# Performance work log

Measured on AMD Instinct MI355X. Metric: run time of the kernel, lower is better.

The kernel has to match this reference:

```python
import jax, jax.numpy as jnp
import numpy as np

N = 50000
E = 1600000
IN_DIM = 128
H = 8
D = 16  # out_dim per head


def setup_inputs() -> dict:
    key = jax.random.key(0)
    ks = jax.random.split(key, 9)
    h = jax.random.normal(ks[0], (N, IN_DIM), dtype=jnp.float32)
    src = jax.random.randint(ks[1], (E,), 0, N, dtype=jnp.int32)
    dst = jax.random.randint(ks[2], (E,), 0, N, dtype=jnp.int32)
    s = 1.0 / np.sqrt(IN_DIM)
    WQ = jax.random.uniform(ks[3], (IN_DIM, H * D), jnp.float32, -s, s)
    WK = jax.random.uniform(ks[4], (IN_DIM, H * D), jnp.float32, -s, s)
    WV = jax.random.uniform(ks[5], (IN_DIM, H * D), jnp.float32, -s, s)
    bQ = jax.random.uniform(ks[6], (H * D,), jnp.float32, -s, s)
    bK = jax.random.uniform(ks[7], (H * D,), jnp.float32, -s, s)
    bV = jax.random.uniform(ks[8], (H * D,), jnp.float32, -s, s)
    return {"h": h, "src": src, "dst": dst, "WQ": WQ, "WK": WK, "WV": WV,
            "bQ": bQ, "bK": bK, "bV": bV}


def reference(h, src, dst, WQ, WK, WV, bQ, bK, bV):
    # Node projections -> [N, H, D]
    Q = (h @ WQ + bQ).reshape(-1, H, D)
    K = (h @ WK + bK).reshape(-1, H, D)
    V = (h @ WV + bV).reshape(-1, H, D)
    # Edge scores: dot(K[src], Q[dst]) per head, scaled+clamped exp -> [E, H]
    scale = jnp.float32(np.sqrt(D))
    score = jnp.exp(jnp.clip(jnp.sum(K[src] * Q[dst], axis=-1) / scale, -5.0, 5.0))
    # Scatter-sum to destination nodes
    wV = jax.ops.segment_sum(score[:, :, None] * V[src], dst, num_segments=N)  # [N, H, D]
    z = jax.ops.segment_sum(score, dst, num_segments=N)  # [N, H]
    return wV / z[:, :, None]
```

## Files before the change

### kernel.cpp

```cpp
#include <hip/hip_runtime.h>

#define N_NODES 50000
#define N_PAD   50048
#define N_EDGES 1600000
#define HD 128
#define CHUNK 4096
#define NCHUNK ((N_EDGES + CHUNK - 1) / CHUNK)
#define NBUCKET ((N_NODES + 127) / 128)

typedef __attribute__((ext_vector_type(8))) short short8;
typedef __attribute__((ext_vector_type(4))) float floatx4;

union U4S8 { uint4 u; short8 s; };

__device__ __forceinline__ unsigned short f2bf(float f) {
    unsigned u = __float_as_uint(f);
    unsigned r = (u + 0x7fffu + ((u >> 16) & 1u)) >> 16;
    return (unsigned short)r;
}

__global__ __launch_bounds__(256) void prep_kernel(
    const float* __restrict__ WQ, const float* __restrict__ WK, const float* __restrict__ WV,
    unsigned short* __restrict__ Wf, int* __restrict__ btot) {
    int bid = blockIdx.x, t = threadIdx.x;
    if (bid < 24) {
        int tid = bid * 256 + t;
        int lane = tid & 63;
        int kstep = (tid >> 6) & 3;
        int ntile = tid >> 8;
        int g = ntile >> 3;
        int c = (ntile & 7) * 16 + (lane & 15);
        int k0 = kstep * 32 + (lane >> 4) * 8;
        const float* W = (g == 0) ? WQ : (g == 1) ? WK : WV;
        unsigned short r[8];
#pragma unroll
        for (int j = 0; j < 8; ++j)
            r[j] = f2bf(W[(size_t)(k0 + j) * HD + c]);
        *(uint4*)(Wf + (size_t)tid * 8) = *(uint4*)r;
    } else {
        int i = (bid - 24) * 256 + t;
        if (i < NBUCKET) btot[i] = 0;
    }
}


__global__ __launch_bounds__(256) void k_chunkhist(const int* __restrict__ dst,
                                                   int* __restrict__ chunkhist,
                                                   int* __restrict__ btot) {
    __shared__ int hist[NBUCKET];
    int t = threadIdx.x, c = blockIdx.x;
    for (int i = t; i < NBUCKET; i += 256) hist[i] = 0;
    __syncthreads();
    int e0 = c * CHUNK;
    int cnt = min(CHUNK, N_EDGES - e0);
    const uint4* d4 = (const uint4*)(dst + e0);
    int cnt4 = cnt >> 2;
    for (int i = t; i < cnt4; i += 256) {
        uint4 v = d4[i];
        atomicAdd(&hist[v.x >> 7], 1);
        atomicAdd(&hist[v.y >> 7], 1);
        atomicAdd(&hist[v.z >> 7], 1);
        atomicAdd(&hist[v.w >> 7], 1);
    }
    __syncthreads();
    for (int i = t; i < NBUCKET; i += 256) {
        int v = hist[i];
        chunkhist[c * NBUCKET + i] = v;
        if (v) atomicAdd(&btot[i], v);
    }
}

__global__ __launch_bounds__(256) void k_choff(const int* __restrict__ chunkhist,
                                               const int* __restrict__ btot,
                                               int* __restrict__ bucket_ptr,
                                               int* __restrict__ chunkoff) {
    int b = blockIdx.x, t = threadIdx.x;
    int x = 0;
    for (int i = t; i < NBUCKET; i += 256)
        if (i < b) x += btot[i];
    __shared__ int red[256];
    red[t] = x;
    __syncthreads();
    for (int off = 128; off > 0; off >>= 1) {
        if (t < off) red[t] += red[t + off];
        __syncthreads();
    }
    int base = red[0];
    if (t == 0) {
        bucket_ptr[b] = base;
        if (b == NBUCKET - 1) bucket_ptr[NBUCKET] = base + btot[b];
    }
    const int PER = (NCHUNK + 255) / 256;
    int c0 = t * PER;
    int v[PER];
    int s = 0;
#pragma unroll
    for (int i = 0; i < PER; ++i) {
        int c = c0 + i;
        v[i] = (c < NCHUNK) ? chunkhist[c * NBUCKET + b] : 0;
        s += v[i];
    }
    __shared__ int part[256];
    part[t] = s;
    __syncthreads();
    for (int off = 1; off < 256; off <<= 1) {
        int y = (t >= off) ? part[t - off] : 0;
        __syncthreads();
        part[t] += y;
        __syncthreads();
    }
    int run = base + part[t] - s;
#pragma unroll
    for (int i = 0; i < PER; ++i) {
        int c = c0 + i;
        if (c < NCHUNK) { chunkoff[c * NBUCKET + b] = run; run += v[i]; }
    }
}

__global__ __launch_bounds__(256) void k_scatter(const int* __restrict__ src,
                                                 const int* __restrict__ dst,
                                                 const int* __restrict__ chunkoff,
                                                 int* __restrict__ packed) {
    __shared__ int cur[NBUCKET];
    int t = threadIdx.x, c = blockIdx.x;
    for (int i = t; i < NBUCKET; i += 256) cur[i] = chunkoff[c * NBUCKET + i];
    __syncthreads();
    int e0 = c * CHUNK;
    int cnt = min(CHUNK, N_EDGES - e0);
    const uint4* d4 = (const uint4*)(dst + e0);
    const uint4* s4 = (const uint4*)(src + e0);
    int cnt4 = cnt >> 2;
    for (int i = t; i < cnt4; i += 256) {
        uint4 d = d4[i];
        uint4 s = s4[i];
        int pos;
        pos = atomicAdd(&cur[d.x >> 7], 1); packed[pos] = (s.x << 7) | (d.x & 127);
        pos = atomicAdd(&cur[d.y >> 7], 1); packed[pos] = (s.y << 7) | (d.y & 127);
        pos = atomicAdd(&cur[d.z >> 7], 1); packed[pos] = (s.z << 7) | (d.z & 127);
        pos = atomicAdd(&cur[d.w >> 7], 1); packed[pos] = (s.w << 7) | (d.w & 127);
    }
}

__global__ __launch_bounds__(256) void k_finalize(const int* __restrict__ bucket_ptr,
                                                  const int* __restrict__ packed,
                                                  int* __restrict__ row_ptr,
                                                  int* __restrict__ col_src) {
    __shared__ int hist[128], part[128], cur[128];
    int b = blockIdx.x, t = threadIdx.x;
    if (t < 128) hist[t] = 0;
    __syncthreads();
    int ebeg = bucket_ptr[b], eend = bucket_ptr[b + 1];
    int m = eend - ebeg;
    for (int i = t; i < m; i += 256)
        atomicAdd(&hist[packed[ebeg + i] & 127], 1);
    __syncthreads();
    int v = 0;
    if (t < 128) { v = hist[t]; part[t] = v; }
    __syncthreads();
    for (int off = 1; off < 128; off <<= 1) {
        int x = 0;
        if (t < 128 && t >= off) x = part[t - off];
        __syncthreads();
        if (t < 128) part[t] += x;
        __syncthreads();
    }
    if (t < 128) {
        int excl = part[t] - v;
        int node = b * 128 + t;
        if (node < N_NODES) row_ptr[node] = ebeg + excl;
        if (node == N_NODES - 1) row_ptr[N_NODES] = eend;
        cur[t] = ebeg + excl;
    }
    __syncthreads();
    for (int i = t; i < m; i += 256) {
        int p = packed[ebeg + i];
        int pos = atomicAdd(&cur[p & 127], 1);
        col_src[pos] = p >> 7;
    }
}


__global__ __launch_bounds__(256) void proj_mfma(
    const float* __restrict__ h, const unsigned short* __restrict__ Wf,
    const float* __restrict__ bQ, const float* __restrict__ bK, const float* __restrict__ bV,
    float* __restrict__ Qo, unsigned short* __restrict__ Kb, unsigned short* __restrict__ Vb) {
    int t = threadIdx.x;
    int w = t >> 6;
    int l = t & 63;
    int m0 = blockIdx.x * 64;
    int nt0 = w * 6;

    floatx4 acc[4][6];
#pragma unroll
    for (int mt = 0; mt < 4; ++mt)
#pragma unroll
        for (int nt = 0; nt < 6; ++nt)
            acc[mt][nt] = (floatx4){0.f, 0.f, 0.f, 0.f};

    int arow = m0 + (l & 15);
    int akoff = (l >> 4) * 8;

#pragma unroll
    for (int kstep = 0; kstep < 4; ++kstep) {
        short8 a[4], b[6];
#pragma unroll
        for (int mt = 0; mt < 4; ++mt) {
            int row = arow + mt * 16;
            unsigned short r[8];
            if (row < N_NODES) {
                const float4* ap = (const float4*)(h + (size_t)row * HD + akoff + kstep * 32);
                float4 f0 = ap[0], f1 = ap[1];
                r[0] = f2bf(f0.x); r[1] = f2bf(f0.y); r[2] = f2bf(f0.z); r[3] = f2bf(f0.w);
                r[4] = f2bf(f1.x); r[5] = f2bf(f1.y); r[6] = f2bf(f1.z); r[7] = f2bf(f1.w);
            } else {
#pragma unroll
                for (int j = 0; j < 8; ++j) r[j] = 0;
            }
            a[mt] = *(short8*)r;
        }
#pragma unroll
        for (int nt = 0; nt < 6; ++nt) {
            U4S8 u;
            u.u = *(const uint4*)(Wf + ((size_t)((nt0 + nt) * 4 + kstep) * 64 + l) * 8);
            b[nt] = u.s;
        }
#pragma unroll
        for (int mt = 0; mt < 4; ++mt)
#pragma unroll
            for (int nt = 0; nt < 6; ++nt)
                acc[mt][nt] = __builtin_amdgcn_mfma_f32_16x16x32_bf16(
                    a[mt], b[nt], acc[mt][nt], 0, 0, 0);
    }

#pragma unroll
    for (int nt = 0; nt < 6; ++nt) {
        int ntile = nt0 + nt;
        int g = ntile >> 3;
        int cc = (ntile & 7) * 16 + (l & 15);
        float bias = (g == 0) ? bQ[cc] : (g == 1) ? bK[cc] : bV[cc];
#pragma unroll
        for (int mt = 0; mt < 4; ++mt) {
#pragma unroll
            for (int r = 0; r < 4; ++r) {
                int grow = m0 + mt * 16 + (l >> 4) * 4 + r;
                if (grow < N_NODES) {
                    float val = acc[mt][nt][r] + bias;
                    if (g == 0)      Qo[(size_t)grow * HD + cc] = val;
                    else if (g == 1) Kb[(size_t)grow * HD + cc] = f2bf(val);
                    else             Vb[(size_t)grow * HD + cc] = f2bf(val);
                }
            }
        }
    }
}


__device__ __forceinline__ float blo(unsigned u) { return __uint_as_float(u << 16); }
__device__ __forceinline__ float bhi(unsigned u) { return __uint_as_float(u & 0xffff0000u); }

__global__ __launch_bounds__(256) void attn_kernel(
    const float* __restrict__ Q,
    const unsigned short* __restrict__ Kb, const unsigned short* __restrict__ Vb,
    const int* __restrict__ row_ptr, const int* __restrict__ col_src,
    float* __restrict__ out) {
    int n = blockIdx.x * 4 + (threadIdx.x >> 6);
    if (n >= N_NODES) return;
    int l = threadIdx.x & 63;
    int o = l >> 3;
    int p = l & 7;

    const float4* Qv = (const float4*)(Q + (size_t)n * HD + p * 16);
    float4 q0 = Qv[0], q1 = Qv[1], q2 = Qv[2], q3 = Qv[3];

    float acc[16];
#pragma unroll
    for (int j = 0; j < 16; ++j) acc[j] = 0.f;
    float z = 0.f;

    int beg = row_ptr[n], end = row_ptr[n + 1];

    for (int base = beg; base < end; base += 64) {
        int mm = min(64, end - base);
        int e_l = col_src[(base + l < end) ? (base + l) : beg];
        int steps = (mm + 7) >> 3;

        int s0 = __shfl(e_l, o);
        const uint4* Kp = (const uint4*)(Kb + (size_t)s0 * HD + p * 16);
        const uint4* Vp = (const uint4*)(Vb + (size_t)s0 * HD + p * 16);
        uint4 ka = Kp[0], kb = Kp[1], va = Vp[0], vb = Vp[1];

        for (int i = 0; i < steps; ++i) {
            uint4 nka = ka, nkb = kb, nva = va, nvb = vb;
            if (i + 1 < steps) {
                int s1 = __shfl(e_l, 8 * (i + 1) + o);
                const uint4* Kn = (const uint4*)(Kb + (size_t)s1 * HD + p * 16);
                const uint4* Vn = (const uint4*)(Vb + (size_t)s1 * HD + p * 16);
                nka = Kn[0]; nkb = Kn[1]; nva = Vn[0]; nvb = Vn[1];
            }
            float dot = blo(ka.x) * q0.x + bhi(ka.x) * q0.y
                      + blo(ka.y) * q0.z + bhi(ka.y) * q0.w
                      + blo(ka.z) * q1.x + bhi(ka.z) * q1.y
                      + blo(ka.w) * q1.z + bhi(ka.w) * q1.w
                      + blo(kb.x) * q2.x + bhi(kb.x) * q2.y
                      + blo(kb.y) * q2.z + bhi(kb.y) * q2.w
                      + blo(kb.z) * q3.x + bhi(kb.z) * q3.y
                      + blo(kb.w) * q3.z + bhi(kb.w) * q3.w;
            float sc = __expf(fminf(fmaxf(dot * 0.25f, -5.f), 5.f));
            if (8 * i + o >= mm) sc = 0.f;
            acc[0]  = fmaf(sc, blo(va.x), acc[0]);
            acc[1]  = fmaf(sc, bhi(va.x), acc[1]);
            acc[2]  = fmaf(sc, blo(va.y), acc[2]);
            acc[3]  = fmaf(sc, bhi(va.y), acc[3]);
            acc[4]  = fmaf(sc, blo(va.z), acc[4]);
            acc[5]  = fmaf(sc, bhi(va.z), acc[5]);
            acc[6]  = fmaf(sc, blo(va.w), acc[6]);
            acc[7]  = fmaf(sc, bhi(va.w), acc[7]);
            acc[8]  = fmaf(sc, blo(vb.x), acc[8]);
            acc[9]  = fmaf(sc, bhi(vb.x), acc[9]);
            acc[10] = fmaf(sc, blo(vb.y), acc[10]);
            acc[11] = fmaf(sc, bhi(vb.y), acc[11]);
            acc[12] = fmaf(sc, blo(vb.z), acc[12]);
            acc[13] = fmaf(sc, bhi(vb.z), acc[13]);
            acc[14] = fmaf(sc, blo(vb.w), acc[14]);
            acc[15] = fmaf(sc, bhi(vb.w), acc[15]);
            z += sc;
            ka = nka; kb = nkb; va = nva; vb = nvb;
        }
    }

#pragma unroll
    for (int j = 0; j < 16; ++j) {
        acc[j] += __shfl_xor(acc[j], 8);
        acc[j] += __shfl_xor(acc[j], 16);
        acc[j] += __shfl_xor(acc[j], 32);
    }
    z += __shfl_xor(z, 8);
    z += __shfl_xor(z, 16);
    z += __shfl_xor(z, 32);

    if (o == 0) {
        float inv = 1.f / z;
        float4* O = (float4*)(out + (size_t)n * HD + p * 16);
        O[0] = (float4){acc[0] * inv,  acc[1] * inv,  acc[2] * inv,  acc[3] * inv};
        O[1] = (float4){acc[4] * inv,  acc[5] * inv,  acc[6] * inv,  acc[7] * inv};
        O[2] = (float4){acc[8] * inv,  acc[9] * inv,  acc[10] * inv, acc[11] * inv};
        O[3] = (float4){acc[12] * inv, acc[13] * inv, acc[14] * inv, acc[15] * inv};
    }
}


static inline char* align256(char* p) {
    return (char*)(((uintptr_t)p + 255) & ~(uintptr_t)255);
}

extern "C" void kernel_launch(void* const* d_in, const int* in_sizes, int n_in,
                              void* d_out, int out_size, void* d_ws, size_t ws_size,
                              hipStream_t stream) {
    const float* h  = (const float*)d_in[0];
    const int*   src = (const int*)d_in[1];
    const int*   dst = (const int*)d_in[2];
    const float* WQ = (const float*)d_in[3];
    const float* WK = (const float*)d_in[4];
    const float* WV = (const float*)d_in[5];
    const float* bQ = (const float*)d_in[6];
    const float* bK = (const float*)d_in[7];
    const float* bV = (const float*)d_in[8];
    float* out = (float*)d_out;

    char* p = (char*)d_ws;
    float* Q = (float*)p;                    p += (size_t)N_PAD * HD * 4;
    unsigned short* Kb = (unsigned short*)p; p += (size_t)N_PAD * HD * 2;
    unsigned short* Vb = (unsigned short*)p; p += (size_t)N_PAD * HD * 2;
    unsigned short* Wf = (unsigned short*)p; p += (size_t)24 * 4 * 64 * 8 * 2;
    p = align256(p);
    int* row_ptr    = (int*)p;               p += (N_NODES + 2) * 4;
    p = align256(p);
    int* bucket_ptr = (int*)p;               p += (NBUCKET + 1) * 4;
    p = align256(p);
    int* btot       = (int*)p;               p += NBUCKET * 4;
    p = align256(p);
    int* chunkhist  = (int*)p;               p += (size_t)NCHUNK * NBUCKET * 4;
    p = align256(p);
    int* chunkoff   = (int*)p;               p += (size_t)NCHUNK * NBUCKET * 4;
    p = align256(p);
    int* packed     = (int*)p;               p += (size_t)N_EDGES * 4;
    p = align256(p);
    int* col_src    = (int*)p;               p += (size_t)N_EDGES * 4;

    prep_kernel<<<26, 256, 0, stream>>>(WQ, WK, WV, Wf, btot);
    k_chunkhist<<<NCHUNK, 256, 0, stream>>>(dst, chunkhist, btot);
    k_choff<<<NBUCKET, 256, 0, stream>>>(chunkhist, btot, bucket_ptr, chunkoff);
    k_scatter<<<NCHUNK, 256, 0, stream>>>(src, dst, chunkoff, packed);
    k_finalize<<<NBUCKET, 256, 0, stream>>>(bucket_ptr, packed, row_ptr, col_src);
    proj_mfma<<<N_PAD / 64, 256, 0, stream>>>(h, Wf, bQ, bK, bV, Q, Kb, Vb);
    attn_kernel<<<(N_NODES + 3) / 4, 256, 0, stream>>>(Q, Kb, Vb, row_ptr, col_src, out);
}
```

Measured before the change: 292.7 us.

## Merge weight prep into histogram kernel, restructure projection tiling, split attention launch

The weight-conversion prep kernel is folded into extra blocks of the chunk histogram kernel, and the bucket-total zeroing moves to a memset. The projection kernel now gives each wave its own 16 rows across all 24 output tiles, instead of a 64x96 register tile per wave. This cuts register pressure but reloads the B fragments per wave. Attention is split into three launches over node ranges, which adds launch overhead and may change cache locality or scheduling.

```diff
diff --git a/kernel.cpp b/kernel.cpp
--- a/kernel.cpp
+++ b/kernel.cpp
@@ -19,36 +19,28 @@
     return (unsigned short)r;
 }
 
-__global__ __launch_bounds__(256) void prep_kernel(
+__global__ __launch_bounds__(256) void k_chunkhist(
+    const int* __restrict__ dst, int* __restrict__ chunkhist, int* __restrict__ btot,
     const float* __restrict__ WQ, const float* __restrict__ WK, const float* __restrict__ WV,
-    unsigned short* __restrict__ Wf, int* __restrict__ btot) {
-    int bid = blockIdx.x, t = threadIdx.x;
-    if (bid < 24) {
-        int tid = bid * 256 + t;
+    unsigned short* __restrict__ Wf) {
+    int t = threadIdx.x, c = blockIdx.x;
+    if (c >= NCHUNK) {
+        int tid = (c - NCHUNK) * 256 + t;
         int lane = tid & 63;
         int kstep = (tid >> 6) & 3;
         int ntile = tid >> 8;
         int g = ntile >> 3;
-        int c = (ntile & 7) * 16 + (lane & 15);
+        int col = (ntile & 7) * 16 + (lane & 15);
         int k0 = kstep * 32 + (lane >> 4) * 8;
         const float* W = (g == 0) ? WQ : (g == 1) ? WK : WV;
         unsigned short r[8];
 #pragma unroll
         for (int j = 0; j < 8; ++j)
-            r[j] = f2bf(W[(size_t)(k0 + j) * HD + c]);
+            r[j] = f2bf(W[(size_t)(k0 + j) * HD + col]);
         *(uint4*)(Wf + (size_t)tid * 8) = *(uint4*)r;
-    } else {
-        int i = (bid - 24) * 256 + t;
-        if (i < NBUCKET) btot[i] = 0;
-    }
-}
-
-
-__global__ __launch_bounds__(256) void k_chunkhist(const int* __restrict__ dst,
-                                                   int* __restrict__ chunkhist,
-                                                   int* __restrict__ btot) {
+        return;
+    }
     __shared__ int hist[NBUCKET];
-    int t = threadIdx.x, c = blockIdx.x;
     for (int i = t; i < NBUCKET; i += 256) hist[i] = 0;
     __syncthreads();
     int e0 = c * CHUNK;
@@ -187,68 +179,48 @@
     int t = threadIdx.x;
     int w = t >> 6;
     int l = t & 63;
-    int m0 = blockIdx.x * 64;
-    int nt0 = w * 6;
-
-    floatx4 acc[4][6];
-#pragma unroll
-    for (int mt = 0; mt < 4; ++mt)
-#pragma unroll
-        for (int nt = 0; nt < 6; ++nt)
-            acc[mt][nt] = (floatx4){0.f, 0.f, 0.f, 0.f};
-
-    int arow = m0 + (l & 15);
+    int row0 = blockIdx.x * 64 + w * 16;
+    int arow = row0 + (l & 15);
     int akoff = (l >> 4) * 8;
-
-#pragma unroll
-    for (int kstep = 0; kstep < 4; ++kstep) {
-        short8 a[4], b[6];
-#pragma unroll
-        for (int mt = 0; mt < 4; ++mt) {
-            int row = arow + mt * 16;
-            unsigned short r[8];
-            if (row < N_NODES) {
-                const float4* ap = (const float4*)(h + (size_t)row * HD + akoff + kstep * 32);
-                float4 f0 = ap[0], f1 = ap[1];
-                r[0] = f2bf(f0.x); r[1] = f2bf(f0.y); r[2] = f2bf(f0.z); r[3] = f2bf(f0.w);
-                r[4] = f2bf(f1.x); r[5] = f2bf(f1.y); r[6] = f2bf(f1.z); r[7] = f2bf(f1.w);
-            } else {
-#pragma unroll
-                for (int j = 0; j < 8; ++j) r[j] = 0;
-            }
-            a[mt] = *(short8*)r;
+    bool rowok = arow < N_NODES;
+
+    short8 a[4];
+#pragma unroll
+    for (int ks = 0; ks < 4; ++ks) {
+        unsigned short r[8];
+        if (rowok) {
+            const float4* ap = (const float4*)(h + (size_t)arow * HD + ks * 32 + akoff);
+            float4 f0 = ap[0], f1 = ap[1];
+            r[0] = f2bf(f0.x); r[1] = f2bf(f0.y); r[2] = f2bf(f0.z); r[3] = f2bf(f0.w);
+            r[4] = f2bf(f1.x); r[5] = f2bf(f1.y); r[6] = f2bf(f1.z); r[7] = f2bf(f1.w);
+        } else {
+#pragma unroll
+            for (int j = 0; j < 8; ++j) r[j] = 0;
         }
-#pragma unroll
-        for (int nt = 0; nt < 6; ++nt) {
+        a[ks] = *(short8*)r;
+    }
+
+    int orow0 = row0 + (l >> 4) * 4;
+#pragma unroll
+    for (int nt = 0; nt < 24; ++nt) {
+        floatx4 acc = (floatx4){0.f, 0.f, 0.f, 0.f};
+#pragma unroll
+        for (int ks = 0; ks < 4; ++ks) {
             U4S8 u;
-            u.u = *(const uint4*)(Wf + ((size_t)((nt0 + nt) * 4 + kstep) * 64 + l) * 8);
-            b[nt] = u.s;
+            u.u = *(const uint4*)(Wf + ((size_t)(nt * 4 + ks) * 64 + l) * 8);
+            acc = __builtin_amdgcn_mfma_f32_16x16x32_bf16(a[ks], u.s, acc, 0, 0, 0);
         }
-#pragma unroll
-        for (int mt = 0; mt < 4; ++mt)
-#pragma unroll
-            for (int nt = 0; nt < 6; ++nt)
-                acc[mt][nt] = __builtin_amdgcn_mfma_f32_16x16x32_bf16(
-                    a[mt], b[nt], acc[mt][nt], 0, 0, 0);
-    }
-
-#pragma unroll
-    for (int nt = 0; nt < 6; ++nt) {
-        int ntile = nt0 + nt;
-        int g = ntile >> 3;
-        int cc = (ntile & 7) * 16 + (l & 15);
+        int g = nt >> 3;
+        int cc = (nt & 7) * 16 + (l & 15);
         float bias = (g == 0) ? bQ[cc] : (g == 1) ? bK[cc] : bV[cc];
 #pragma unroll
-        for (int mt = 0; mt < 4; ++mt) {
-#pragma unroll
-            for (int r = 0; r < 4; ++r) {
-                int grow = m0 + mt * 16 + (l >> 4) * 4 + r;
-                if (grow < N_NODES) {
-                    float val = acc[mt][nt][r] + bias;
-                    if (g == 0)      Qo[(size_t)grow * HD + cc] = val;
-                    else if (g == 1) Kb[(size_t)grow * HD + cc] = f2bf(val);
-                    else             Vb[(size_t)grow * HD + cc] = f2bf(val);
-                }
+        for (int r = 0; r < 4; ++r) {
+            int grow = orow0 + r;
+            if (grow < N_NODES) {
+                float val = acc[r] + bias;
+                if (g == 0)      Qo[(size_t)grow * HD + cc] = val;
+                else if (g == 1) Kb[(size_t)grow * HD + cc] = f2bf(val);
+                else             Vb[(size_t)grow * HD + cc] = f2bf(val);
             }
         }
     }
@@ -262,9 +234,9 @@
     const float* __restrict__ Q,
     const unsigned short* __restrict__ Kb, const unsigned short* __restrict__ Vb,
     const int* __restrict__ row_ptr, const int* __restrict__ col_src,
-    float* __restrict__ out) {
-    int n = blockIdx.x * 4 + (threadIdx.x >> 6);
-    if (n >= N_NODES) return;
+    float* __restrict__ out, int nbase, int nend) {
+    int n = nbase + blockIdx.x * 4 + (threadIdx.x >> 6);
+    if (n >= nend) return;
     int l = threadIdx.x & 63;
     int o = l >> 3;
     int p = l & 7;
@@ -387,11 +359,14 @@
     p = align256(p);
     int* col_src    = (int*)p;               p += (size_t)N_EDGES * 4;
 
-    prep_kernel<<<26, 256, 0, stream>>>(WQ, WK, WV, Wf, btot);
-    k_chunkhist<<<NCHUNK, 256, 0, stream>>>(dst, chunkhist, btot);
+    (void)hipMemsetAsync(btot, 0, NBUCKET * sizeof(int), stream);
+    k_chunkhist<<<NCHUNK + 24, 256, 0, stream>>>(dst, chunkhist, btot, WQ, WK, WV, Wf);
     k_choff<<<NBUCKET, 256, 0, stream>>>(chunkhist, btot, bucket_ptr, chunkoff);
     k_scatter<<<NCHUNK, 256, 0, stream>>>(src, dst, chunkoff, packed);
     k_finalize<<<NBUCKET, 256, 0, stream>>>(bucket_ptr, packed, row_ptr, col_src);
     proj_mfma<<<N_PAD / 64, 256, 0, stream>>>(h, Wf, bQ, bK, bV, Q, Kb, Vb);
-    attn_kernel<<<(N_NODES + 3) / 4, 256, 0, stream>>>(Q, Kb, Vb, row_ptr, col_src, out);
-}
+    const int T1 = 16668, T2 = 33336;
+    attn_kernel<<<(T1 + 3) / 4, 256, 0, stream>>>(Q, Kb, Vb, row_ptr, col_src, out, 0, T1);
+    attn_kernel<<<(T2 - T1 + 3) / 4, 256, 0, stream>>>(Q, Kb, Vb, row_ptr, col_src, out, T1, T2);
+    attn_kernel<<<(N_NODES - T2 + 3) / 4, 256, 0, stream>>>(Q, Kb, Vb, row_ptr, col_src, out, T2, N_NODES);
+}
```

Measured after the change: 269.5 us. -7.9%, faster.
